# Optimization experiments

Hardware: AMD Instinct MI355X
Metric: run time of the kernel (lower is better)

The kernel has to match this reference:

```python
import jax, jax.numpy as jnp
import numpy as np

B, S, D, H, DFF = 2, 2048, 1024, 16, 4096
DK = D // H
EPS = 1e-6
MASK_FILL = -1.0  # original code uses -1**9 == -1 (precedence bug), NOT -1e9


def layernorm(x, gamma, beta):
    # original: (x - mean) / (std + eps), std unbiased (torch default ddof=1), scalar gamma/beta
    mean = jnp.mean(x, axis=-1, keepdims=True)
    std = jnp.std(x, axis=-1, keepdims=True, ddof=1)
    return gamma * (x - mean) / (std + EPS) + beta


def setup_inputs() -> dict:
    key = jax.random.key(0)
    ks = jax.random.split(key, 12)
    sc = 0.02
    return {
        "x": jax.random.normal(ks[0], (B, S, D), jnp.float32),
        "src_mask": jnp.ones((B, 1, 1, S), jnp.int32),
        "wq": jax.random.normal(ks[1], (D, D), jnp.float32) * sc,
        "bq": jnp.zeros((D,), jnp.float32),
        "wk": jax.random.normal(ks[2], (D, D), jnp.float32) * sc,
        "bk": jnp.zeros((D,), jnp.float32),
        "wv": jax.random.normal(ks[3], (D, D), jnp.float32) * sc,
        "bv": jnp.zeros((D,), jnp.float32),
        "wo": jax.random.normal(ks[4], (D, D), jnp.float32) * sc,
        "bo": jnp.zeros((D,), jnp.float32),
        "w1": jax.random.normal(ks[5], (D, DFF), jnp.float32) * sc,
        "b1": jnp.zeros((DFF,), jnp.float32),
        "w2": jax.random.normal(ks[6], (DFF, D), jnp.float32) * sc,
        "b2": jnp.zeros((D,), jnp.float32),
        "g1": jnp.ones((), jnp.float32),
        "be1": jnp.zeros((), jnp.float32),
        "g2": jnp.ones((), jnp.float32),
        "be2": jnp.zeros((), jnp.float32),
    }


def reference(x, src_mask, wq, bq, wk, bk, wv, bv, wo, bo,
              w1, b1, w2, b2, g1, be1, g2, be2):
    # --- residual 1: pre-LN self-attention ---
    xn = layernorm(x, g1, be1)
    q = (xn @ wq + bq).reshape(B, S, H, DK).transpose(0, 2, 1, 3)  # [B,H,S,DK]
    k = (xn @ wk + bk).reshape(B, S, H, DK).transpose(0, 2, 1, 3)
    v = (xn @ wv + bv).reshape(B, S, H, DK).transpose(0, 2, 1, 3)
    scores = jnp.einsum('bhqd,bhkd->bhqk', q, k) / jnp.sqrt(jnp.float32(DK))
    scores = jnp.where(src_mask == 0, MASK_FILL, scores)
    attn = jax.nn.softmax(scores, axis=-1)
    ctx = jnp.einsum('bhqk,bhkd->bhqd', attn, v)
    ctx = ctx.transpose(0, 2, 1, 3).reshape(B, S, D)
    attn_out = ctx @ wo + bo
    x = x + attn_out  # dropout is identity in eval

    # --- residual 2: pre-LN feed-forward ---
    xn = layernorm(x, g2, be2)
    h = jax.nn.relu(xn @ w1 + b1)
    ff_out = h @ w2 + b2
    return x + ff_out
```

## Files before the change

### kernel.cpp

```cpp
#include <hip/hip_runtime.h>

typedef unsigned short u16;
typedef __bf16 bf16x8 __attribute__((ext_vector_type(8)));
typedef float f32x4 __attribute__((ext_vector_type(4)));

#define AS1U(p) ((__attribute__((address_space(1))) unsigned int*)(p))
#define AS3U(p) ((__attribute__((address_space(3))) unsigned int*)(p))

__device__ __forceinline__ u16 f2bf(float f) {
  union { float f; unsigned int i; } c; c.f = f;
  return (u16)((c.i + 0x7FFFu + ((c.i >> 16) & 1u)) >> 16);
}
__device__ __forceinline__ u16 f2bf_trunc(float f) {
  union { float f; unsigned int i; } c; c.f = f;
  return (u16)(c.i >> 16);
}

template <int BM, int BN, int OMODE>
__global__ __launch_bounds__(256) void gemm_bt(
    const u16* __restrict__ A, long lda,
    const u16* __restrict__ B, long ldb,
    void* __restrict__ Cv, long ldc,
    int K, float scale, const float* __restrict__ bias,
    const float* __restrict__ res, long ldres, int relu) {
  constexpr int BK = 32;
  constexpr int WN = (BN == 128) ? 64 : 32;
  constexpr int MI = 4, NJ = WN / 16;
  __shared__ u16 As0[BM * BK], As1[BM * BK];
  __shared__ u16 Bs0[BN * BK], Bs1[BN * BK];
  const int t = threadIdx.x;
  const int w = t >> 6, l = t & 63;
  const int wr = w >> 1, wc = w & 1;
  const int quad = l >> 4, mlo = l & 15;
  const long row0 = (long)blockIdx.x * BM;
  const long col0 = (long)blockIdx.y * BN;

  f32x4 acc[MI][NJ] = {};

  auto stage = [&](u16 (&Ad)[BM * BK], u16 (&Bd)[BN * BK], int k0) {
#pragma unroll
    for (int i = 0; i < BM / 64; i++) {
      int s = t + i * 256, r = s >> 2, c = s & 3;
      const u16* g = A + (row0 + r) * lda + k0 + (c ^ (r & 3)) * 8;
      __builtin_amdgcn_global_load_lds(AS1U(g), AS3U(&Ad[s * 8]), 16, 0, 0);
    }
#pragma unroll
    for (int i = 0; i < BN / 64; i++) {
      int s = t + i * 256, r = s >> 2, c = s & 3;
      const u16* g = B + (col0 + r) * ldb + k0 + (c ^ (r & 3)) * 8;
      __builtin_amdgcn_global_load_lds(AS1U(g), AS3U(&Bd[s * 8]), 16, 0, 0);
    }
  };
  auto compute = [&](const u16 (&Asr)[BM * BK], const u16 (&Bsr)[BN * BK]) {
    bf16x8 a[MI], b[NJ];
#pragma unroll
    for (int i = 0; i < MI; i++) {
      int r = wr * 64 + i * 16 + mlo;
      a[i] = *(const bf16x8*)&Asr[(r * 4 + (quad ^ (mlo & 3))) * 8];
    }
#pragma unroll
    for (int j = 0; j < NJ; j++) {
      int r = wc * WN + j * 16 + mlo;
      b[j] = *(const bf16x8*)&Bsr[(r * 4 + (quad ^ (mlo & 3))) * 8];
    }
#pragma unroll
    for (int i = 0; i < MI; i++)
#pragma unroll
      for (int j = 0; j < NJ; j++)
        acc[i][j] = __builtin_amdgcn_mfma_f32_16x16x32_bf16(a[i], b[j], acc[i][j], 0, 0, 0);
  };

  stage(As0, Bs0, 0);
  for (int k0 = 0; k0 < K; k0 += 2 * BK) {
    __syncthreads();
    stage(As1, Bs1, k0 + BK);
    compute(As0, Bs0);
    __syncthreads();
    if (k0 + 2 * BK < K) stage(As0, Bs0, k0 + 2 * BK);
    compute(As1, Bs1);
  }

#pragma unroll
  for (int i = 0; i < MI; i++) {
#pragma unroll
    for (int j = 0; j < NJ; j++) {
      const long gn = col0 + wc * WN + j * 16 + mlo;
      const float bv = bias ? bias[gn] : 0.0f;
#pragma unroll
      for (int r = 0; r < 4; r++) {
        const long gm = row0 + wr * 64 + i * 16 + quad * 4 + r;
        float v = acc[i][j][r] * scale + bv;
        if (relu && v < 0.0f) v = 0.0f;
        if (res) v += res[gm * ldres + gn];
        if (OMODE == 0) ((float*)Cv)[gm * ldc + gn] = v;
        else ((u16*)Cv)[gm * ldc + gn] = f2bf(v);
      }
    }
  }
}

__global__ __launch_bounds__(256) void flash_attn(
    const u16* __restrict__ QKV, const u16* __restrict__ VT,
    const int* __restrict__ mask, u16* __restrict__ ctx) {
  __shared__ u16 Qs[128 * 64];
  __shared__ u16 Ks[2][64 * 64];
  __shared__ u16 Vs[2][64 * 64];
  __shared__ u16 Ps[128 * 64];
  const int t = threadIdx.x;
  const int w = t >> 6, l = t & 63;
  const int quad = l >> 4, mlo = l & 15;
  const int z = blockIdx.z, b = z >> 4, h = z & 15;
  const long q0 = (long)blockIdx.x * 128;
  const u16* Qg = QKV + (long)b * (2048L * 3072) + h * 64;
  const u16* Kg = Qg + 1024;
  const u16* Vg = VT + (long)b * (1024L * 2048) + (long)(h * 64) * 2048;
  const int* mrow = mask + b * 2048;

#pragma unroll
  for (int i = 0; i < 4; i++) {
    int s = t + i * 256, r = s >> 3, c = s & 7;
    const u16* g = Qg + (q0 + r) * 3072 + (c ^ (r & 7)) * 8;
    __builtin_amdgcn_global_load_lds(AS1U(g), AS3U(&Qs[s * 8]), 16, 0, 0);
  }
#pragma unroll
  for (int i = 0; i < 2; i++) {
    int s = t + i * 256, r = s >> 3, c = s & 7;
    __builtin_amdgcn_global_load_lds(AS1U(Kg + (long)r * 3072 + (c ^ (r & 7)) * 8),
                                     AS3U(&Ks[0][s * 8]), 16, 0, 0);
    __builtin_amdgcn_global_load_lds(AS1U(Vg + (long)r * 2048 + (c ^ (r & 7)) * 8),
                                     AS3U(&Vs[0][s * 8]), 16, 0, 0);
  }

  f32x4 o[2][5] = {};
  bf16x8 aq[2][2];
  union { u16 s[8]; bf16x8 v; } ones;
#pragma unroll
  for (int e = 0; e < 8; e++) ones.s[e] = 0x3F80;

  for (int it = 0; it < 32; ++it) {
    const int cur = it & 1;
    const int key0 = it * 64;
    __syncthreads();
    if (it == 0) {
#pragma unroll
      for (int i = 0; i < 2; i++)
#pragma unroll
        for (int kk = 0; kk < 2; kk++) {
          int row = w * 32 + i * 16 + mlo;
          aq[i][kk] = *(const bf16x8*)&Qs[(row * 8 + ((kk * 4 + quad) ^ (mlo & 7))) * 8];
        }
    }
    int mz[4];
#pragma unroll
    for (int j = 0; j < 4; j++) mz[j] = mrow[key0 + j * 16 + mlo];
    f32x4 sa[2][4] = {};
#pragma unroll
    for (int kk = 0; kk < 2; kk++) {
      bf16x8 bk[4];
#pragma unroll
      for (int j = 0; j < 4; j++) {
        int rr = j * 16 + mlo;
        bk[j] = *(const bf16x8*)&Ks[cur][(rr * 8 + ((kk * 4 + quad) ^ (mlo & 7))) * 8];
      }
#pragma unroll
      for (int i = 0; i < 2; i++)
#pragma unroll
        for (int j = 0; j < 4; j++)
          sa[i][j] = __builtin_amdgcn_mfma_f32_16x16x32_bf16(aq[i][kk], bk[j], sa[i][j], 0, 0, 0);
    }
#pragma unroll
    for (int i = 0; i < 2; i++)
#pragma unroll
      for (int j = 0; j < 4; j++)
#pragma unroll
        for (int r = 0; r < 4; r++) {
          float s = (mz[j] == 0) ? -1.0f : sa[i][j][r] * 0.125f;
          float p = __expf(s);
          int row = w * 32 + i * 16 + quad * 4 + r;
          int col = j * 16 + mlo;
          Ps[row * 64 + (((col >> 3) ^ (row & 7)) << 3) + (col & 7)] = f2bf_trunc(p);
        }
    __syncthreads();
    if (it + 1 < 32) {
      const int nb = 1 - cur;
      const u16* Kg2 = Kg + (long)(it + 1) * 64 * 3072;
      const u16* Vg2 = Vg + (it + 1) * 64;
#pragma unroll
      for (int i2 = 0; i2 < 2; i2++) {
        int s = t + i2 * 256, r = s >> 3, c = s & 7;
        __builtin_amdgcn_global_load_lds(AS1U(Kg2 + (long)r * 3072 + (c ^ (r & 7)) * 8),
                                         AS3U(&Ks[nb][s * 8]), 16, 0, 0);
        __builtin_amdgcn_global_load_lds(AS1U(Vg2 + (long)r * 2048 + (c ^ (r & 7)) * 8),
                                         AS3U(&Vs[nb][s * 8]), 16, 0, 0);
      }
    }
#pragma unroll
    for (int kk = 0; kk < 2; kk++) {
      bf16x8 ap[2], bv[4];
#pragma unroll
      for (int i = 0; i < 2; i++) {
        int row = w * 32 + i * 16 + mlo;
        ap[i] = *(const bf16x8*)&Ps[(row * 8 + ((kk * 4 + quad) ^ (mlo & 7))) * 8];
      }
#pragma unroll
      for (int j = 0; j < 4; j++) {
        int rr = j * 16 + mlo;
        bv[j] = *(const bf16x8*)&Vs[cur][(rr * 8 + ((kk * 4 + quad) ^ (mlo & 7))) * 8];
      }
#pragma unroll
      for (int i = 0; i < 2; i++) {
#pragma unroll
        for (int j = 0; j < 4; j++)
          o[i][j] = __builtin_amdgcn_mfma_f32_16x16x32_bf16(ap[i], bv[j], o[i][j], 0, 0, 0);
        o[i][4] = __builtin_amdgcn_mfma_f32_16x16x32_bf16(ap[i], ones.v, o[i][4], 0, 0, 0);
      }
    }
  }
  u16* cb = ctx + (long)b * (2048L * 1024) + q0 * 1024 + h * 64;
#pragma unroll
  for (int i = 0; i < 2; i++)
#pragma unroll
    for (int r = 0; r < 4; r++) {
      float inv = 1.0f / o[i][4][r];
      int row = w * 32 + i * 16 + quad * 4 + r;
#pragma unroll
      for (int j = 0; j < 4; j++)
        cb[(long)row * 1024 + j * 16 + mlo] = f2bf(o[i][j][r] * inv);
    }
}

__global__ __launch_bounds__(256) void ln_kernel(const float* __restrict__ x, u16* __restrict__ y,
                                                 const float* __restrict__ g, const float* __restrict__ b) {
  const long row = blockIdx.x;
  const float* xr = x + row * 1024;
  float v[4];
  float s = 0.f, sq = 0.f;
#pragma unroll
  for (int i = 0; i < 4; i++) {
    float f = xr[threadIdx.x + i * 256];
    v[i] = f; s += f; sq += f * f;
  }
#pragma unroll
  for (int o = 32; o > 0; o >>= 1) { s += __shfl_xor(s, o, 64); sq += __shfl_xor(sq, o, 64); }
  __shared__ float ss[4], s2[4];
  const int w = threadIdx.x >> 6;
  if ((threadIdx.x & 63) == 0) { ss[w] = s; s2[w] = sq; }
  __syncthreads();
  s = ss[0] + ss[1] + ss[2] + ss[3];
  sq = s2[0] + s2[1] + s2[2] + s2[3];
  const float mean = s * (1.0f / 1024.0f);
  float var = (sq - s * mean) * (1.0f / 1023.0f);
  var = fmaxf(var, 0.0f);
  const float sc = g[0] / (sqrtf(var) + 1e-6f);
  const float be = b[0];
#pragma unroll
  for (int i = 0; i < 4; i++)
    y[row * 1024 + threadIdx.x + i * 256] = f2bf((v[i] - mean) * sc + be);
}

__global__ __launch_bounds__(256) void ttransb(const float* __restrict__ in, long ldin,
                                               u16* __restrict__ out, long ldo) {
  __shared__ float tile[32][33];
  const int bx = blockIdx.x * 32, by = blockIdx.y * 32;
  const int tx = threadIdx.x & 31, ty = threadIdx.x >> 5;
#pragma unroll
  for (int i = 0; i < 32; i += 8) tile[ty + i][tx] = in[(long)(by + ty + i) * ldin + bx + tx];
  __syncthreads();
#pragma unroll
  for (int i = 0; i < 32; i += 8)
    out[(long)(bx + ty + i) * ldo + by + tx] = f2bf(tile[tx][ty + i]);
}

__global__ __launch_bounds__(256) void ttrans1(const u16* __restrict__ in, long ldin, long siz,
                                               u16* __restrict__ out, long ldo, long soz) {
  __shared__ u16 tile[32][33];
  const long zi = (long)blockIdx.z * siz, zo = (long)blockIdx.z * soz;
  const int bx = blockIdx.x * 32, by = blockIdx.y * 32;
  const int tx = threadIdx.x & 31, ty = threadIdx.x >> 5;
#pragma unroll
  for (int i = 0; i < 32; i += 8)
    tile[ty + i][tx] = in[zi + (long)(by + ty + i) * ldin + bx + tx];
  __syncthreads();
#pragma unroll
  for (int i = 0; i < 32; i += 8)
    out[zo + (long)(bx + ty + i) * ldo + by + tx] = tile[tx][ty + i];
}

__global__ __launch_bounds__(256) void concat3(const float* __restrict__ a, const float* __restrict__ b,
                                               const float* __restrict__ c, float* __restrict__ o) {
  const int i = blockIdx.x * 256 + threadIdx.x;
  o[i] = (i < 1024) ? a[i] : ((i < 2048) ? b[i - 1024] : c[i - 2048]);
}

extern "C" void kernel_launch(void* const* d_in, const int* in_sizes, int n_in,
                              void* d_out, int out_size, void* d_ws, size_t ws_size,
                              hipStream_t stream) {
  const float* x   = (const float*)d_in[0];
  const int*   msk = (const int*)d_in[1];
  const float* wq  = (const float*)d_in[2];
  const float* bq  = (const float*)d_in[3];
  const float* wk  = (const float*)d_in[4];
  const float* bk  = (const float*)d_in[5];
  const float* wv  = (const float*)d_in[6];
  const float* bv  = (const float*)d_in[7];
  const float* wo  = (const float*)d_in[8];
  const float* bo  = (const float*)d_in[9];
  const float* w1  = (const float*)d_in[10];
  const float* b1  = (const float*)d_in[11];
  const float* w2  = (const float*)d_in[12];
  const float* b2  = (const float*)d_in[13];
  const float* g1  = (const float*)d_in[14];
  const float* be1 = (const float*)d_in[15];
  const float* g2  = (const float*)d_in[16];
  const float* be2 = (const float*)d_in[17];
  float* out = (float*)d_out;

  char* basep = (char*)d_ws;
  size_t off = 0;
  auto au = [&](size_t nelem) -> u16* {
    u16* r = (u16*)(basep + off);
    off += ((nelem * 2) + 255) & ~(size_t)255;
    return r;
  };
  auto afp = [&](size_t nelem) -> float* {
    float* r = (float*)(basep + off);
    off += ((nelem * 4) + 255) & ~(size_t)255;
    return r;
  };

  u16* xnH  = au((size_t)4096 * 1024);
  u16* QKV  = au((size_t)4096 * 3072);
  u16* VTH  = au((size_t)2 * 1024 * 2048);
  u16* ctxH = au((size_t)4096 * 1024);
  float* x1 = afp((size_t)4096 * 1024);
  u16* hb   = au((size_t)4096 * 4096);
  u16* WqkvT = au((size_t)3072 * 1024);
  u16* woT  = au((size_t)1024 * 1024);
  u16* w1T  = au((size_t)4096 * 1024);
  u16* w2T  = au((size_t)1024 * 4096);
  float* biasQKV = afp(3072);

  const dim3 blk(256);

  ln_kernel<<<4096, blk, 0, stream>>>(x, xnH, g1, be1);

  ttransb<<<dim3(32, 32), blk, 0, stream>>>(wq, 1024, WqkvT, 1024);
  ttransb<<<dim3(32, 32), blk, 0, stream>>>(wk, 1024, WqkvT + (size_t)1024 * 1024, 1024);
  ttransb<<<dim3(32, 32), blk, 0, stream>>>(wv, 1024, WqkvT + (size_t)2048 * 1024, 1024);
  concat3<<<12, blk, 0, stream>>>(bq, bk, bv, biasQKV);

  gemm_bt<128, 128, 2><<<dim3(32, 24), blk, 0, stream>>>(
      xnH, 1024, WqkvT, 1024, QKV, 3072, 1024, 1.0f,
      biasQKV, (const float*)0, 0, 0);

  ttrans1<<<dim3(32, 64, 2), blk, 0, stream>>>(
      QKV + 2048, 3072, (long)2048 * 3072, VTH, 2048, (long)1024 * 2048);

  flash_attn<<<dim3(16, 1, 32), blk, 0, stream>>>(QKV, VTH, msk, ctxH);

  ttransb<<<dim3(32, 32), blk, 0, stream>>>(wo, 1024, woT, 1024);
  gemm_bt<128, 64, 0><<<dim3(32, 16), blk, 0, stream>>>(
      ctxH, 1024, woT, 1024, x1, 1024, 1024, 1.0f, bo, x, 1024, 0);

  ln_kernel<<<4096, blk, 0, stream>>>(x1, xnH, g2, be2);

  ttransb<<<dim3(128, 32), blk, 0, stream>>>(w1, 4096, w1T, 1024);
  gemm_bt<128, 128, 2><<<dim3(32, 32), blk, 0, stream>>>(
      xnH, 1024, w1T, 1024, hb, 4096, 1024, 1.0f,
      b1, (const float*)0, 0, 1);

  ttransb<<<dim3(32, 128), blk, 0, stream>>>(w2, 1024, w2T, 4096);
  gemm_bt<128, 64, 0><<<dim3(32, 16), blk, 0, stream>>>(
      hb, 4096, w2T, 4096, out, 1024, 4096, 1.0f, b2, x1, 1024, 0);
}
```

Baseline: 398.6 us.

## Compute transposed scores so P tile is written with packed LDS stores

The attention kernel now computes S^T (K as the A operand, Q as the B operand), so each lane holds four consecutive keys for one query. It converts them to bf16 and writes them to the P tile as one packed 8-byte store with an XOR swizzle, replacing sixteen scalar 2-byte LDS writes. The mask is read as int4 vectors. The loop is also reordered so there is a single barrier per iteration, with the next K/V prefetch issued before the score computation. Because the P buffer is now reused across iterations with only one barrier, there is a possible hazard if waves fall out of step.

```diff
diff --git a/kernel.cpp b/kernel.cpp
--- a/kernel.cpp
+++ b/kernel.cpp
@@ -10,10 +10,6 @@
 __device__ __forceinline__ u16 f2bf(float f) {
   union { float f; unsigned int i; } c; c.f = f;
   return (u16)((c.i + 0x7FFFu + ((c.i >> 16) & 1u)) >> 16);
-}
-__device__ __forceinline__ u16 f2bf_trunc(float f) {
-  union { float f; unsigned int i; } c; c.f = f;
-  return (u16)(c.i >> 16);
 }
 
 template <int BM, int BN, int OMODE>
@@ -131,55 +127,15 @@
                                      AS3U(&Vs[0][s * 8]), 16, 0, 0);
   }
 
-  f32x4 o[2][5] = {};
-  bf16x8 aq[2][2];
+  f32x4 o[2][4] = {};
+  f32x4 den[2] = {};
+  bf16x8 bq[2][2];
   union { u16 s[8]; bf16x8 v; } ones;
 #pragma unroll
   for (int e = 0; e < 8; e++) ones.s[e] = 0x3F80;
 
   for (int it = 0; it < 32; ++it) {
     const int cur = it & 1;
-    const int key0 = it * 64;
-    __syncthreads();
-    if (it == 0) {
-#pragma unroll
-      for (int i = 0; i < 2; i++)
-#pragma unroll
-        for (int kk = 0; kk < 2; kk++) {
-          int row = w * 32 + i * 16 + mlo;
-          aq[i][kk] = *(const bf16x8*)&Qs[(row * 8 + ((kk * 4 + quad) ^ (mlo & 7))) * 8];
-        }
-    }
-    int mz[4];
-#pragma unroll
-    for (int j = 0; j < 4; j++) mz[j] = mrow[key0 + j * 16 + mlo];
-    f32x4 sa[2][4] = {};
-#pragma unroll
-    for (int kk = 0; kk < 2; kk++) {
-      bf16x8 bk[4];
-#pragma unroll
-      for (int j = 0; j < 4; j++) {
-        int rr = j * 16 + mlo;
-        bk[j] = *(const bf16x8*)&Ks[cur][(rr * 8 + ((kk * 4 + quad) ^ (mlo & 7))) * 8];
-      }
-#pragma unroll
-      for (int i = 0; i < 2; i++)
-#pragma unroll
-        for (int j = 0; j < 4; j++)
-          sa[i][j] = __builtin_amdgcn_mfma_f32_16x16x32_bf16(aq[i][kk], bk[j], sa[i][j], 0, 0, 0);
-    }
-#pragma unroll
-    for (int i = 0; i < 2; i++)
-#pragma unroll
-      for (int j = 0; j < 4; j++)
-#pragma unroll
-        for (int r = 0; r < 4; r++) {
-          float s = (mz[j] == 0) ? -1.0f : sa[i][j][r] * 0.125f;
-          float p = __expf(s);
-          int row = w * 32 + i * 16 + quad * 4 + r;
-          int col = j * 16 + mlo;
-          Ps[row * 64 + (((col >> 3) ^ (row & 7)) << 3) + (col & 7)] = f2bf_trunc(p);
-        }
     __syncthreads();
     if (it + 1 < 32) {
       const int nb = 1 - cur;
@@ -194,38 +150,88 @@
                                          AS3U(&Vs[nb][s * 8]), 16, 0, 0);
       }
     }
+    if (it == 0) {
+#pragma unroll
+      for (int jq = 0; jq < 2; jq++)
+#pragma unroll
+        for (int kk = 0; kk < 2; kk++) {
+          int row = w * 32 + jq * 16 + mlo;
+          bq[jq][kk] = *(const bf16x8*)&Qs[(row * 8 + ((kk * 4 + quad) ^ (row & 7))) * 8];
+        }
+    }
+    f32x4 sa[4][2] = {};
+#pragma unroll
+    for (int kk = 0; kk < 2; kk++) {
+      bf16x8 ak[4];
+#pragma unroll
+      for (int i = 0; i < 4; i++) {
+        int row = i * 16 + mlo;
+        ak[i] = *(const bf16x8*)&Ks[cur][(row * 8 + ((kk * 4 + quad) ^ (row & 7))) * 8];
+      }
+#pragma unroll
+      for (int i = 0; i < 4; i++)
+#pragma unroll
+        for (int jq = 0; jq < 2; jq++)
+          sa[i][jq] = __builtin_amdgcn_mfma_f32_16x16x32_bf16(ak[i], bq[jq][kk], sa[i][jq], 0, 0, 0);
+    }
+    const int4* m4 = (const int4*)(mrow + it * 64);
+#pragma unroll
+    for (int i = 0; i < 4; i++) {
+      const int4 mi = m4[i * 4 + quad];
+#pragma unroll
+      for (int jq = 0; jq < 2; jq++) {
+        float p0 = __expf(mi.x == 0 ? -1.0f : sa[i][jq][0] * 0.125f);
+        float p1 = __expf(mi.y == 0 ? -1.0f : sa[i][jq][1] * 0.125f);
+        float p2 = __expf(mi.z == 0 ? -1.0f : sa[i][jq][2] * 0.125f);
+        float p3 = __expf(mi.w == 0 ? -1.0f : sa[i][jq][3] * 0.125f);
+        union { float f; unsigned u; } a0, a1, a2, a3;
+        a0.f = p0; a1.f = p1; a2.f = p2; a3.f = p3;
+        uint2 pk;
+        pk.x = (a0.u >> 16) | (a1.u & 0xFFFF0000u);
+        pk.y = (a2.u >> 16) | (a3.u & 0xFFFF0000u);
+        int row = w * 32 + jq * 16 + mlo;
+        int g = (i * 4 + quad) ^ mlo;
+        *(uint2*)&Ps[row * 64 + g * 4] = pk;
+      }
+    }
 #pragma unroll
     for (int kk = 0; kk < 2; kk++) {
       bf16x8 ap[2], bv[4];
 #pragma unroll
-      for (int i = 0; i < 2; i++) {
-        int row = w * 32 + i * 16 + mlo;
-        ap[i] = *(const bf16x8*)&Ps[(row * 8 + ((kk * 4 + quad) ^ (mlo & 7))) * 8];
-      }
-#pragma unroll
-      for (int j = 0; j < 4; j++) {
-        int rr = j * 16 + mlo;
-        bv[j] = *(const bf16x8*)&Vs[cur][(rr * 8 + ((kk * 4 + quad) ^ (mlo & 7))) * 8];
-      }
-#pragma unroll
-      for (int i = 0; i < 2; i++) {
-#pragma unroll
-        for (int j = 0; j < 4; j++)
-          o[i][j] = __builtin_amdgcn_mfma_f32_16x16x32_bf16(ap[i], bv[j], o[i][j], 0, 0, 0);
-        o[i][4] = __builtin_amdgcn_mfma_f32_16x16x32_bf16(ap[i], ones.v, o[i][4], 0, 0, 0);
+      for (int i_q = 0; i_q < 2; i_q++) {
+        int row = w * 32 + i_q * 16 + mlo;
+        int g0 = (kk * 8 + quad * 2) ^ mlo;
+        int g1 = (kk * 8 + quad * 2 + 1) ^ mlo;
+        union { unsigned u[4]; bf16x8 v; } apu;
+        uint2 ua = *(const uint2*)&Ps[row * 64 + g0 * 4];
+        uint2 ub = *(const uint2*)&Ps[row * 64 + g1 * 4];
+        apu.u[0] = ua.x; apu.u[1] = ua.y; apu.u[2] = ub.x; apu.u[3] = ub.y;
+        ap[i_q] = apu.v;
+      }
+#pragma unroll
+      for (int jd = 0; jd < 4; jd++) {
+        int row = jd * 16 + mlo;
+        bv[jd] = *(const bf16x8*)&Vs[cur][(row * 8 + ((kk * 4 + quad) ^ (row & 7))) * 8];
+      }
+#pragma unroll
+      for (int i_q = 0; i_q < 2; i_q++) {
+#pragma unroll
+        for (int jd = 0; jd < 4; jd++)
+          o[i_q][jd] = __builtin_amdgcn_mfma_f32_16x16x32_bf16(ap[i_q], bv[jd], o[i_q][jd], 0, 0, 0);
+        den[i_q] = __builtin_amdgcn_mfma_f32_16x16x32_bf16(ap[i_q], ones.v, den[i_q], 0, 0, 0);
       }
     }
   }
   u16* cb = ctx + (long)b * (2048L * 1024) + q0 * 1024 + h * 64;
 #pragma unroll
-  for (int i = 0; i < 2; i++)
+  for (int i_q = 0; i_q < 2; i_q++)
 #pragma unroll
     for (int r = 0; r < 4; r++) {
-      float inv = 1.0f / o[i][4][r];
-      int row = w * 32 + i * 16 + quad * 4 + r;
-#pragma unroll
-      for (int j = 0; j < 4; j++)
-        cb[(long)row * 1024 + j * 16 + mlo] = f2bf(o[i][j][r] * inv);
+      const float inv = 1.0f / den[i_q][r];
+      const int row = w * 32 + i_q * 16 + quad * 4 + r;
+#pragma unroll
+      for (int jd = 0; jd < 4; jd++)
+        cb[(long)row * 1024 + jd * 16 + mlo] = f2bf(o[i_q][jd][r] * inv);
     }
 }
 
```

Result: slower. 414.0 us (+3.9%).

## Prefetch K/V earlier in attention loop and fuse prep kernels into one launch

Applied to the files above, without the earlier changes.

In the flash-attention loop, the next K/V tile prefetch now starts right after the top-of-iteration barrier. The barrier between writing P and running the PV matmul is removed, which gives the loads more time to overlap with the QK^T and softmax work and drops one barrier per iteration. Separately, the first layernorm, all six weight transpose/casts and the QKV bias concat are merged into a single prep_kernel launch dispatched by block index. This cuts kernel-launch count and lets the independent prep work run concurrently. Correctness now relies on each wave reading only its own P rows, and on the in-flight prefetch not interfering with waits on the current buffer.

```diff
diff --git a/kernel.cpp b/kernel.cpp
--- a/kernel.cpp
+++ b/kernel.cpp
@@ -141,6 +141,19 @@
     const int cur = it & 1;
     const int key0 = it * 64;
     __syncthreads();
+    if (it + 1 < 32) {
+      const int nb = 1 - cur;
+      const u16* Kg2 = Kg + (long)(it + 1) * 64 * 3072;
+      const u16* Vg2 = Vg + (it + 1) * 64;
+#pragma unroll
+      for (int i2 = 0; i2 < 2; i2++) {
+        int s = t + i2 * 256, r = s >> 3, c = s & 7;
+        __builtin_amdgcn_global_load_lds(AS1U(Kg2 + (long)r * 3072 + (c ^ (r & 7)) * 8),
+                                         AS3U(&Ks[nb][s * 8]), 16, 0, 0);
+        __builtin_amdgcn_global_load_lds(AS1U(Vg2 + (long)r * 2048 + (c ^ (r & 7)) * 8),
+                                         AS3U(&Vs[nb][s * 8]), 16, 0, 0);
+      }
+    }
     if (it == 0) {
 #pragma unroll
       for (int i = 0; i < 2; i++)
@@ -180,20 +193,6 @@
           int col = j * 16 + mlo;
           Ps[row * 64 + (((col >> 3) ^ (row & 7)) << 3) + (col & 7)] = f2bf_trunc(p);
         }
-    __syncthreads();
-    if (it + 1 < 32) {
-      const int nb = 1 - cur;
-      const u16* Kg2 = Kg + (long)(it + 1) * 64 * 3072;
-      const u16* Vg2 = Vg + (it + 1) * 64;
-#pragma unroll
-      for (int i2 = 0; i2 < 2; i2++) {
-        int s = t + i2 * 256, r = s >> 3, c = s & 7;
-        __builtin_amdgcn_global_load_lds(AS1U(Kg2 + (long)r * 3072 + (c ^ (r & 7)) * 8),
-                                         AS3U(&Ks[nb][s * 8]), 16, 0, 0);
-        __builtin_amdgcn_global_load_lds(AS1U(Vg2 + (long)r * 2048 + (c ^ (r & 7)) * 8),
-                                         AS3U(&Vs[nb][s * 8]), 16, 0, 0);
-      }
-    }
 #pragma unroll
     for (int kk = 0; kk < 2; kk++) {
       bf16x8 ap[2], bv[4];
@@ -229,9 +228,9 @@
     }
 }
 
-__global__ __launch_bounds__(256) void ln_kernel(const float* __restrict__ x, u16* __restrict__ y,
-                                                 const float* __restrict__ g, const float* __restrict__ b) {
-  const long row = blockIdx.x;
+__device__ __forceinline__ void ln_row(const float* __restrict__ x, u16* __restrict__ y,
+                                       const float* __restrict__ g, const float* __restrict__ b,
+                                       long row, float* ss, float* s2) {
   const float* xr = x + row * 1024;
   float v[4];
   float s = 0.f, sq = 0.f;
@@ -242,7 +241,6 @@
   }
 #pragma unroll
   for (int o = 32; o > 0; o >>= 1) { s += __shfl_xor(s, o, 64); sq += __shfl_xor(sq, o, 64); }
-  __shared__ float ss[4], s2[4];
   const int w = threadIdx.x >> 6;
   if ((threadIdx.x & 63) == 0) { ss[w] = s; s2[w] = sq; }
   __syncthreads();
@@ -258,10 +256,39 @@
     y[row * 1024 + threadIdx.x + i * 256] = f2bf((v[i] - mean) * sc + be);
 }
 
-__global__ __launch_bounds__(256) void ttransb(const float* __restrict__ in, long ldin,
-                                               u16* __restrict__ out, long ldo) {
+__global__ __launch_bounds__(256) void ln_kernel(const float* __restrict__ x, u16* __restrict__ y,
+                                                 const float* __restrict__ g, const float* __restrict__ b) {
+  __shared__ float ss[4], s2[4];
+  ln_row(x, y, g, b, blockIdx.x, ss, s2);
+}
+
+__global__ __launch_bounds__(256) void prep_kernel(
+    const float* __restrict__ x, const float* __restrict__ g1, const float* __restrict__ be1,
+    const float* __restrict__ wq, const float* __restrict__ wk, const float* __restrict__ wv,
+    const float* __restrict__ wo, const float* __restrict__ w1, const float* __restrict__ w2,
+    const float* __restrict__ bq, const float* __restrict__ bk, const float* __restrict__ bv,
+    u16* __restrict__ xnH, u16* __restrict__ WqkvT, u16* __restrict__ woT,
+    u16* __restrict__ w1T, u16* __restrict__ w2T, float* __restrict__ biasQKV) {
   __shared__ float tile[32][33];
-  const int bx = blockIdx.x * 32, by = blockIdx.y * 32;
+  __shared__ float ss[4], s2[4];
+  const int bid = blockIdx.x;
+  if (bid >= 12300) {
+    ln_row(x, xnH, g1, be1, bid - 12300, ss, s2);
+    return;
+  }
+  if (bid >= 12288) {
+    const int i = (bid - 12288) * 256 + threadIdx.x;
+    if (i < 3072) biasQKV[i] = (i < 1024) ? bq[i] : ((i < 2048) ? bk[i - 1024] : bv[i - 2048]);
+    return;
+  }
+  const float* in; u16* out; long ldin, ldo; int ti, tiles_x;
+  if (bid < 1024)      { in = wq; out = WqkvT;                     ldin = 1024; ldo = 1024; ti = bid;        tiles_x = 32; }
+  else if (bid < 2048) { in = wk; out = WqkvT + (size_t)1024*1024; ldin = 1024; ldo = 1024; ti = bid - 1024; tiles_x = 32; }
+  else if (bid < 3072) { in = wv; out = WqkvT + (size_t)2048*1024; ldin = 1024; ldo = 1024; ti = bid - 2048; tiles_x = 32; }
+  else if (bid < 4096) { in = wo; out = woT;                       ldin = 1024; ldo = 1024; ti = bid - 3072; tiles_x = 32; }
+  else if (bid < 8192) { in = w1; out = w1T;                       ldin = 4096; ldo = 1024; ti = bid - 4096; tiles_x = 128; }
+  else                 { in = w2; out = w2T;                       ldin = 1024; ldo = 4096; ti = bid - 8192; tiles_x = 32; }
+  const int bx = (ti % tiles_x) * 32, by = (ti / tiles_x) * 32;
   const int tx = threadIdx.x & 31, ty = threadIdx.x >> 5;
 #pragma unroll
   for (int i = 0; i < 32; i += 8) tile[ty + i][tx] = in[(long)(by + ty + i) * ldin + bx + tx];
@@ -284,12 +311,6 @@
 #pragma unroll
   for (int i = 0; i < 32; i += 8)
     out[zo + (long)(bx + ty + i) * ldo + by + tx] = tile[tx][ty + i];
-}
-
-__global__ __launch_bounds__(256) void concat3(const float* __restrict__ a, const float* __restrict__ b,
-                                               const float* __restrict__ c, float* __restrict__ o) {
-  const int i = blockIdx.x * 256 + threadIdx.x;
-  o[i] = (i < 1024) ? a[i] : ((i < 2048) ? b[i - 1024] : c[i - 2048]);
 }
 
 extern "C" void kernel_launch(void* const* d_in, const int* in_sizes, int n_in,
@@ -342,12 +363,8 @@
 
   const dim3 blk(256);
 
-  ln_kernel<<<4096, blk, 0, stream>>>(x, xnH, g1, be1);
-
-  ttransb<<<dim3(32, 32), blk, 0, stream>>>(wq, 1024, WqkvT, 1024);
-  ttransb<<<dim3(32, 32), blk, 0, stream>>>(wk, 1024, WqkvT + (size_t)1024 * 1024, 1024);
-  ttransb<<<dim3(32, 32), blk, 0, stream>>>(wv, 1024, WqkvT + (size_t)2048 * 1024, 1024);
-  concat3<<<12, blk, 0, stream>>>(bq, bk, bv, biasQKV);
+  prep_kernel<<<16396, blk, 0, stream>>>(x, g1, be1, wq, wk, wv, wo, w1, w2,
+                                         bq, bk, bv, xnH, WqkvT, woT, w1T, w2T, biasQKV);
 
   gemm_bt<128, 128, 2><<<dim3(32, 24), blk, 0, stream>>>(
       xnH, 1024, WqkvT, 1024, QKV, 3072, 1024, 1.0f,
@@ -358,18 +375,15 @@
 
   flash_attn<<<dim3(16, 1, 32), blk, 0, stream>>>(QKV, VTH, msk, ctxH);
 
-  ttransb<<<dim3(32, 32), blk, 0, stream>>>(wo, 1024, woT, 1024);
   gemm_bt<128, 64, 0><<<dim3(32, 16), blk, 0, stream>>>(
       ctxH, 1024, woT, 1024, x1, 1024, 1024, 1.0f, bo, x, 1024, 0);
 
   ln_kernel<<<4096, blk, 0, stream>>>(x1, xnH, g2, be2);
 
-  ttransb<<<dim3(128, 32), blk, 0, stream>>>(w1, 4096, w1T, 1024);
   gemm_bt<128, 128, 2><<<dim3(32, 32), blk, 0, stream>>>(
       xnH, 1024, w1T, 1024, hb, 4096, 1024, 1.0f,
       b1, (const float*)0, 0, 1);
 
-  ttransb<<<dim3(32, 128), blk, 0, stream>>>(w2, 1024, w2T, 4096);
   gemm_bt<128, 64, 0><<<dim3(32, 16), blk, 0, stream>>>(
       hb, 4096, w2T, 4096, out, 1024, 4096, 1.0f, b2, x1, 1024, 0);
 }
```

Result: faster. 389.2 us (-2.4%).
